# Kernel optimization log

Hardware: AMD Instinct MI355X
Metric: run time of the kernel (lower is better)

Reference implementation:

```python
import jax, jax.numpy as jnp
import numpy as np

B, S, E, H = 4, 1024, 768, 8
HD = E // H
FF = 4 * E
SCALING = HD ** -0.5


def _layernorm(x, g, b, eps=1e-5):
    m = jnp.mean(x, axis=-1, keepdims=True)
    v = jnp.var(x, axis=-1, keepdims=True)
    return (x - m) / jnp.sqrt(v + eps) * g + b


def setup_inputs() -> dict:
    key = jax.random.key(0)
    ks = jax.random.split(key, 12)
    w = lambda k, shp: (jax.random.normal(k, shp, jnp.float32) * 0.02)
    return {
        "x": jax.random.normal(ks[0], (B, S, E), jnp.float32),
        "dist_map": jax.random.uniform(ks[1], (B, H, S, S), jnp.float32),
        "mask": jnp.zeros((B, S), jnp.int32),
        "Wq": w(ks[2], (E, E)), "bq": jnp.zeros((E,), jnp.float32),
        "Wk": w(ks[3], (E, E)), "bk": jnp.zeros((E,), jnp.float32),
        "Wv": w(ks[4], (E, E)), "bv": jnp.zeros((E,), jnp.float32),
        "Wo": w(ks[5], (E, E)), "bo": jnp.zeros((E,), jnp.float32),
        "ln1_g": jnp.ones((E,), jnp.float32), "ln1_b": jnp.zeros((E,), jnp.float32),
        "W1": w(ks[6], (FF, E)), "b1": jnp.zeros((FF,), jnp.float32),
        "W2": w(ks[7], (E, FF)), "b2": jnp.zeros((E,), jnp.float32),
        "ln2_g": jnp.ones((E,), jnp.float32), "ln2_b": jnp.zeros((E,), jnp.float32),
    }


def reference(x, dist_map, mask, Wq, bq, Wk, bk, Wv, bv, Wo, bo,
              ln1_g, ln1_b, W1, b1, W2, b2, ln2_g, ln2_b):
    # --- attention residual block (pre-norm) ---
    h = _layernorm(x, ln1_g, ln1_b)
    # NOTE: torch does .view(B, H, S, HD) directly on [B, S, E] -> pure reshape, no transpose
    q = (h @ Wq.T + bq).reshape(B, H, S, HD)
    k = (h @ Wk.T + bk).reshape(B, H, S, HD)
    v = (h @ Wv.T + bv).reshape(B, H, S, HD)
    attn_weights = jnp.einsum("bhqd,bhkd->bhqk", q, k)
    pad = mask.astype(bool)[:, None, None, :]          # [B,1,1,S]
    attn_weights = jnp.where(pad, -10000.0, attn_weights)  # mask BEFORE scaling (as in source)
    probs = jax.nn.softmax(attn_weights * SCALING, axis=-1)
    probs = (probs + dist_map) * 0.5                   # post-softmax dist bias
    ctx = jnp.einsum("bhal,bhlv->bhav", probs, v)      # [B,H,S,HD]
    ctx = ctx.transpose(0, 2, 1, 3).reshape(B, S, E)
    x1 = x + (ctx @ Wo.T + bo)
    # --- FFN residual block (pre-norm) ---
    h2 = _layernorm(x1, ln2_g, ln2_b)
    ffn = jax.nn.gelu(h2 @ W1.T + b1, approximate=False) @ W2.T + b2
    out = x1 + ffn
    return out, probs
```

## Files before the change

kernel.cpp:

```cpp
#include <hip/hip_runtime.h>
#include <math.h>

typedef unsigned short u16;
typedef u16   u16x8  __attribute__((ext_vector_type(8)));
typedef u16   u16x4  __attribute__((ext_vector_type(4)));
typedef __bf16 bf16x8 __attribute__((ext_vector_type(8)));
typedef float f32x4  __attribute__((ext_vector_type(4)));

#define SZ_BSE   3145728
#define HEADSZ   98304
#define SCALING  0.10206207261596577f

__device__ __forceinline__ u16 f2bf(float f) {
  union { float f; unsigned u; } c; c.f = f;
  unsigned u = c.u;
  return (u16)((u + 0x7fffu + ((u >> 16) & 1u)) >> 16);
}

typedef const __attribute__((address_space(1))) unsigned int* gas1_t;
typedef __attribute__((address_space(3))) unsigned int* las3_t;
__device__ __forceinline__ void gload16(const void* g, void* l) {
  __builtin_amdgcn_global_load_lds((gas1_t)g, (las3_t)l, 16, 0, 0);
}

__global__ __launch_bounds__(256) void cvt_k(const float* __restrict__ in,
                                             u16* __restrict__ out, int n) {
  int i = (blockIdx.x * 256 + threadIdx.x) * 4;
  if (i >= n) return;
  f32x4 v = *(const f32x4*)&in[i];
  u16x4 o; o[0]=f2bf(v[0]); o[1]=f2bf(v[1]); o[2]=f2bf(v[2]); o[3]=f2bf(v[3]);
  *(u16x4*)&out[i] = o;
}

__global__ __launch_bounds__(256) void ln_k(const float* __restrict__ x,
                                            const float* __restrict__ g,
                                            const float* __restrict__ b,
                                            u16* __restrict__ out) {
  const int row = blockIdx.x;
  const float* xr = x + (long)row * 768;
  const int t = threadIdx.x;
  float v0 = xr[t], v1 = xr[t + 256], v2 = xr[t + 512];
  float s = v0 + v1 + v2, ss = v0*v0 + v1*v1 + v2*v2;
  for (int o = 32; o > 0; o >>= 1) { s += __shfl_xor(s, o); ss += __shfl_xor(ss, o); }
  __shared__ float red[8];
  int w = t >> 6;
  if ((t & 63) == 0) { red[w] = s; red[w + 4] = ss; }
  __syncthreads();
  s  = red[0] + red[1] + red[2] + red[3];
  ss = red[4] + red[5] + red[6] + red[7];
  float mean = s * (1.0f / 768.0f);
  float var  = ss * (1.0f / 768.0f) - mean * mean;
  float rstd = rsqrtf(var + 1e-5f);
  u16* orow = out + (long)row * 768;
  orow[t]       = f2bf((v0 - mean) * rstd * g[t]       + b[t]);
  orow[t + 256] = f2bf((v1 - mean) * rstd * g[t + 256] + b[t + 256]);
  orow[t + 512] = f2bf((v2 - mean) * rstd * g[t + 512] + b[t + 512]);
}

__global__ __launch_bounds__(256) void softmax_k(float* __restrict__ sc,
                                                 const float* __restrict__ dist) {
  const long row = blockIdx.x;
  float* sr = sc + row * 1024;
  const float* dr = dist + row * 1024;
  const int t = threadIdx.x;
  f32x4 x = *(const f32x4*)&sr[t * 4];
  x[0] *= SCALING; x[1] *= SCALING; x[2] *= SCALING; x[3] *= SCALING;
  float m = fmaxf(fmaxf(x[0], x[1]), fmaxf(x[2], x[3]));
  for (int o = 32; o > 0; o >>= 1) m = fmaxf(m, __shfl_xor(m, o));
  __shared__ float red[8];
  int w = t >> 6;
  if ((t & 63) == 0) red[w] = m;
  __syncthreads();
  m = fmaxf(fmaxf(red[0], red[1]), fmaxf(red[2], red[3]));
  f32x4 e;
  e[0] = expf(x[0] - m); e[1] = expf(x[1] - m);
  e[2] = expf(x[2] - m); e[3] = expf(x[3] - m);
  float s = e[0] + e[1] + e[2] + e[3];
  for (int o = 32; o > 0; o >>= 1) s += __shfl_xor(s, o);
  if ((t & 63) == 0) red[w + 4] = s;
  __syncthreads();
  s = red[4] + red[5] + red[6] + red[7];
  float inv = 1.0f / s;
  f32x4 d = *(const f32x4*)&dr[t * 4];
  f32x4 o4;
  o4[0] = (e[0] * inv + d[0]) * 0.5f;
  o4[1] = (e[1] * inv + d[1]) * 0.5f;
  o4[2] = (e[2] * inv + d[2]) * 0.5f;
  o4[3] = (e[3] * inv + d[3]) * 0.5f;
  *(f32x4*)&sr[t * 4] = o4;
}

__global__ __launch_bounds__(256) void vtrans_k(const u16* __restrict__ v,
                                                u16* __restrict__ vt) {
  __shared__ u16 tile[64 * 98];
  const int z = blockIdx.x >> 4;
  const int s0 = (blockIdx.x & 15) << 6;
  const int t = threadIdx.x;
  const u16* src = v + (long)z * HEADSZ + (long)s0 * 96;
#pragma unroll
  for (int it = 0; it < 3; ++it) {
    int i = it * 2048 + t * 8;
    int s = i / 96, d = i % 96;
    *(u16x8*)&tile[s * 98 + d] = *(const u16x8*)&src[i];
  }
  __syncthreads();
  u16* dst = vt + (long)z * HEADSZ + s0;
#pragma unroll
  for (int it = 0; it < 6; ++it) {
    int o = it * 1024 + t * 4;
    int d = o >> 6, s = o & 63;
    u16x4 wv;
#pragma unroll
    for (int j = 0; j < 4; ++j) wv[j] = tile[(s + j) * 98 + d];
    *(u16x4*)&dst[(long)d * 1024 + s] = wv;
  }
}

__global__ __launch_bounds__(256) void reduce_k(const float* __restrict__ p,
                                                const float* __restrict__ resid,
                                                const float* __restrict__ bias,
                                                float* __restrict__ out) {
  long i = ((long)blockIdx.x * 256 + threadIdx.x) * 4;
  f32x4 a = *(const f32x4*)&p[i];
  f32x4 b = *(const f32x4*)&p[3145728 + i];
  f32x4 c = *(const f32x4*)&p[6291456 + i];
  f32x4 r = *(const f32x4*)&resid[i];
  int cb = (int)(i % 768);
  f32x4 g = *(const f32x4*)&bias[cb];
  f32x4 o;
  o[0] = r[0] + g[0] + a[0] + b[0] + c[0];
  o[1] = r[1] + g[1] + a[1] + b[1] + c[1];
  o[2] = r[2] + g[2] + a[2] + b[2] + c[2];
  o[3] = r[3] + g[3] + a[3] + b[3] + c[3];
  *(f32x4*)&out[i] = o;
}

enum { EPI_QKV = 0, EPI_SCORES = 1, EPI_PV = 2, EPI_GELU = 3, EPI_PARTIAL = 4 };

template <int EPI, bool AF32>
__global__ __launch_bounds__(256, 2)
void gemm_k(const void* __restrict__ Av, long sAz, int lda,
            const u16* __restrict__ W, long sWz, int ldw,
            void* __restrict__ Cv, long sCz, int ldc,
            const float* __restrict__ bias,
            const int* __restrict__ mask,
            int N, int K, int kchunks) {
  __shared__ u16 sA[4096];
  __shared__ u16 sB[4096];

  const int t  = threadIdx.x;
  const int z  = blockIdx.z;
  const int bz = z / kchunks;
  const int kc = z - bz * kchunks;
  const int klen = K / kchunks;
  const int kbeg = kc * klen, kend = kbeg + klen;
  const int m0 = blockIdx.x * 128;
  const int n0 = blockIdx.y * 128;

  const int r0 = t >> 2;
  const int c0 = (t & 3) << 3;
  char* lA = (char*)sA + ((t >> 6) << 10);
  char* lB = (char*)sB + ((t >> 6) << 10);

  int bn0 = n0 + r0;      if (bn0 > N - 1) bn0 = N - 1;
  int bn1 = n0 + 64 + r0; if (bn1 > N - 1) bn1 = N - 1;
  const u16* Wz  = W + (long)bz * sWz;
  const u16* gB0 = Wz + (long)bn0 * ldw + c0;
  const u16* gB1 = Wz + (long)bn1 * ldw + c0;

  const u16*   Ab = AF32 ? nullptr : (const u16*)Av + (long)bz * sAz;
  const float* Af = AF32 ? (const float*)Av + (long)bz * sAz : nullptr;
  const u16* gA0 = AF32 ? nullptr : Ab + (long)(m0 + r0) * lda + c0;
  const u16* gA1 = AF32 ? nullptr : gA0 + 64 * lda;
  const float* Ap = AF32 ? Af + (long)(m0 + (t >> 1)) * lda + ((t & 1) << 4) : nullptr;
  u16* aw = &sA[(t >> 1) * 32 + ((t & 1) << 4)];

  const int lane = t & 63;
  const int w  = t >> 6;
  const int wm = (w >> 1) * 64, wn = (w & 1) * 64;
  const int lr = lane & 15, lg = lane >> 4;

  f32x4 acc[4][4] = {};

  for (int k0 = kbeg; k0 < kend; k0 += 32) {
    if (AF32) {
      f32x4 a0 = *(const f32x4*)(Ap + k0);
      f32x4 a1 = *(const f32x4*)(Ap + k0 + 4);
      f32x4 a2 = *(const f32x4*)(Ap + k0 + 8);
      f32x4 a3 = *(const f32x4*)(Ap + k0 + 12);
      u16x8 p0, p1;
      p0[0]=f2bf(a0[0]); p0[1]=f2bf(a0[1]); p0[2]=f2bf(a0[2]); p0[3]=f2bf(a0[3]);
      p0[4]=f2bf(a1[0]); p0[5]=f2bf(a1[1]); p0[6]=f2bf(a1[2]); p0[7]=f2bf(a1[3]);
      p1[0]=f2bf(a2[0]); p1[1]=f2bf(a2[1]); p1[2]=f2bf(a2[2]); p1[3]=f2bf(a2[3]);
      p1[4]=f2bf(a3[0]); p1[5]=f2bf(a3[1]); p1[6]=f2bf(a3[2]); p1[7]=f2bf(a3[3]);
      *(u16x8*)aw       = p0;
      *(u16x8*)(aw + 8) = p1;
    } else {
      gload16(gA0 + k0, lA);
      gload16(gA1 + k0, lA + 4096);
    }
    gload16(gB0 + k0, lB);
    gload16(gB1 + k0, lB + 4096);
    __syncthreads();

    bf16x8 aF[4], bF[4];
#pragma unroll
    for (int mi = 0; mi < 4; ++mi)
      aF[mi] = *(const bf16x8*)&sA[(wm + mi * 16 + lr) * 32 + lg * 8];
#pragma unroll
    for (int ni = 0; ni < 4; ++ni)
      bF[ni] = *(const bf16x8*)&sB[(wn + ni * 16 + lr) * 32 + lg * 8];
#pragma unroll
    for (int mi = 0; mi < 4; ++mi)
#pragma unroll
      for (int ni = 0; ni < 4; ++ni)
        acc[mi][ni] = __builtin_amdgcn_mfma_f32_16x16x32_bf16(aF[mi], bF[ni], acc[mi][ni], 0, 0, 0);
    __syncthreads();
  }

  long coff;
  if (EPI == EPI_PV)           coff = (long)(bz >> 3) * 786432 + (long)(bz & 7) * 96;
  else if (EPI == EPI_PARTIAL) coff = (long)kc * sCz;
  else                         coff = (long)bz * sCz;

#pragma unroll
  for (int mi = 0; mi < 4; ++mi) {
#pragma unroll
    for (int ni = 0; ni < 4; ++ni) {
      int gc = n0 + wn + ni * 16 + lr;
      if (gc >= N) continue;
      int gr0 = m0 + wm + mi * 16 + lg * 4;
#pragma unroll
      for (int r = 0; r < 4; ++r) {
        float vv = acc[mi][ni][r];
        long idx = coff + (long)(gr0 + r) * ldc + gc;
        if (EPI == EPI_QKV) {
          vv += bias[gc];
          int wsel = gc >= 1536 ? 2 : (gc >= 768 ? 1 : 0);
          int c = gc - wsel * 768;
          ((u16*)Cv)[(long)wsel * 3145728 + (long)(gr0 + r) * 768 + c] = f2bf(vv);
        } else if (EPI == EPI_SCORES) {
          if (mask[(bz >> 3) * 1024 + gc] != 0) vv = -10000.0f;
          ((float*)Cv)[idx] = vv;
        } else if (EPI == EPI_PV) {
          ((u16*)Cv)[idx] = f2bf(vv);
        } else if (EPI == EPI_GELU) {
          vv += bias[gc];
          vv = 0.5f * vv * (1.0f + erff(vv * 0.70710678118654752f));
          ((u16*)Cv)[idx] = f2bf(vv);
        } else {
          ((float*)Cv)[idx] = vv;
        }
      }
    }
  }
}

extern "C" void kernel_launch(void* const* d_in, const int* in_sizes, int n_in,
                              void* d_out, int out_size, void* d_ws, size_t ws_size,
                              hipStream_t stream) {
  (void)in_sizes; (void)n_in; (void)out_size; (void)ws_size;
  const float* x    = (const float*)d_in[0];
  const float* dist = (const float*)d_in[1];
  const int*   mask = (const int*)d_in[2];
  const float* Wq = (const float*)d_in[3];  const float* bq  = (const float*)d_in[4];
  const float* Wk = (const float*)d_in[5];  const float* bk  = (const float*)d_in[6];
  const float* Wv = (const float*)d_in[7];  const float* bv  = (const float*)d_in[8];
  const float* Wo = (const float*)d_in[9];  const float* bo  = (const float*)d_in[10];
  const float* g1 = (const float*)d_in[11]; const float* b1n = (const float*)d_in[12];
  const float* W1 = (const float*)d_in[13]; const float* b1f = (const float*)d_in[14];
  const float* W2 = (const float*)d_in[15]; const float* b2f = (const float*)d_in[16];
  const float* g2 = (const float*)d_in[17]; const float* b2n = (const float*)d_in[18];

  char* ws = (char*)d_ws;
  u16*   h    = (u16*)(ws + 0);
  u16*   ctx  = (u16*)(ws + 0);
  u16*   qkv  = (u16*)(ws + 6291456);
  u16*   q    = qkv;
  u16*   k    = (u16*)(ws + 12582912);
  u16*   v    = (u16*)(ws + 18874368);
  u16*   vT   = (u16*)(ws + 25165824);
  float* part = (float*)(ws + 6291456);
  u16*   h2   = (u16*)(ws + 31457280);
  u16*   ffn1 = (u16*)(ws + 44040192);
  float* x1   = (float*)(ws + 69206016);
  u16*   wqkvb= (u16*)(ws + 81788928);
  u16*   wob  = (u16*)(ws + 85327872);
  u16*   w1b  = (u16*)(ws + 86507520);
  u16*   w2b  = (u16*)(ws + 91226112);
  float* bqkv = (float*)(ws + 95944704);

  float* outp   = (float*)d_out;
  float* scores = outp + SZ_BSE;

  cvt_k<<<576,  256, 0, stream>>>(Wq, wqkvb,           589824);
  cvt_k<<<576,  256, 0, stream>>>(Wk, wqkvb + 589824,  589824);
  cvt_k<<<576,  256, 0, stream>>>(Wv, wqkvb + 1179648, 589824);
  cvt_k<<<576,  256, 0, stream>>>(Wo, wob, 589824);
  cvt_k<<<2304, 256, 0, stream>>>(W1, w1b, 2359296);
  cvt_k<<<2304, 256, 0, stream>>>(W2, w2b, 2359296);
  hipMemcpyAsync(bqkv,        bq, 3072, hipMemcpyDeviceToDevice, stream);
  hipMemcpyAsync(bqkv + 768,  bk, 3072, hipMemcpyDeviceToDevice, stream);
  hipMemcpyAsync(bqkv + 1536, bv, 3072, hipMemcpyDeviceToDevice, stream);

  ln_k<<<4096, 256, 0, stream>>>(x, g1, b1n, h);

  gemm_k<EPI_QKV, false><<<dim3(32, 18, 1), 256, 0, stream>>>(
      h, 0, 768, wqkvb, 0, 768, qkv, 0, 768, bqkv, nullptr, 2304, 768, 1);

  vtrans_k<<<512, 256, 0, stream>>>(v, vT);

  gemm_k<EPI_SCORES, false><<<dim3(8, 8, 32), 256, 0, stream>>>(
      q, HEADSZ, 96, k, HEADSZ, 96, scores, 1048576, 1024, nullptr, mask, 1024, 96, 1);

  softmax_k<<<32768, 256, 0, stream>>>(scores, dist);

  gemm_k<EPI_PV, true><<<dim3(8, 1, 32), 256, 0, stream>>>(
      scores, 1048576, 1024, vT, HEADSZ, 1024, ctx, 0, 768, nullptr, nullptr, 96, 1024, 1);

  gemm_k<EPI_PARTIAL, false><<<dim3(32, 6, 3), 256, 0, stream>>>(
      ctx, 0, 768, wob, 0, 768, part, 3145728, 768, nullptr, nullptr, 768, 768, 3);
  reduce_k<<<3072, 256, 0, stream>>>(part, x, bo, x1);

  ln_k<<<4096, 256, 0, stream>>>(x1, g2, b2n, h2);

  gemm_k<EPI_GELU, false><<<dim3(32, 24, 1), 256, 0, stream>>>(
      h2, 0, 768, w1b, 0, 768, ffn1, 0, 3072, b1f, nullptr, 3072, 768, 1);

  gemm_k<EPI_PARTIAL, false><<<dim3(32, 6, 3), 256, 0, stream>>>(
      ffn1, 0, 3072, w2b, 0, 3072, part, 3145728, 768, nullptr, nullptr, 768, 3072, 3);
  reduce_k<<<3072, 256, 0, stream>>>(part, x1, b2f, outp);
}
```

Before: 324.2 us.

## Fuse scores, softmax, dist bias and PV into a two-pass attention kernel

```diff
diff --git a/kernel.cpp b/kernel.cpp
--- a/kernel.cpp
+++ b/kernel.cpp
@@ -57,39 +57,6 @@
   orow[t + 512] = f2bf((v2 - mean) * rstd * g[t + 512] + b[t + 512]);
 }
 
-__global__ __launch_bounds__(256) void softmax_k(float* __restrict__ sc,
-                                                 const float* __restrict__ dist) {
-  const long row = blockIdx.x;
-  float* sr = sc + row * 1024;
-  const float* dr = dist + row * 1024;
-  const int t = threadIdx.x;
-  f32x4 x = *(const f32x4*)&sr[t * 4];
-  x[0] *= SCALING; x[1] *= SCALING; x[2] *= SCALING; x[3] *= SCALING;
-  float m = fmaxf(fmaxf(x[0], x[1]), fmaxf(x[2], x[3]));
-  for (int o = 32; o > 0; o >>= 1) m = fmaxf(m, __shfl_xor(m, o));
-  __shared__ float red[8];
-  int w = t >> 6;
-  if ((t & 63) == 0) red[w] = m;
-  __syncthreads();
-  m = fmaxf(fmaxf(red[0], red[1]), fmaxf(red[2], red[3]));
-  f32x4 e;
-  e[0] = expf(x[0] - m); e[1] = expf(x[1] - m);
-  e[2] = expf(x[2] - m); e[3] = expf(x[3] - m);
-  float s = e[0] + e[1] + e[2] + e[3];
-  for (int o = 32; o > 0; o >>= 1) s += __shfl_xor(s, o);
-  if ((t & 63) == 0) red[w + 4] = s;
-  __syncthreads();
-  s = red[4] + red[5] + red[6] + red[7];
-  float inv = 1.0f / s;
-  f32x4 d = *(const f32x4*)&dr[t * 4];
-  f32x4 o4;
-  o4[0] = (e[0] * inv + d[0]) * 0.5f;
-  o4[1] = (e[1] * inv + d[1]) * 0.5f;
-  o4[2] = (e[2] * inv + d[2]) * 0.5f;
-  o4[3] = (e[3] * inv + d[3]) * 0.5f;
-  *(f32x4*)&sr[t * 4] = o4;
-}
-
 __global__ __launch_bounds__(256) void vtrans_k(const u16* __restrict__ v,
                                                 u16* __restrict__ vt) {
   __shared__ u16 tile[64 * 98];
@@ -135,23 +102,162 @@
   *(f32x4*)&out[i] = o;
 }
 
-enum { EPI_QKV = 0, EPI_SCORES = 1, EPI_PV = 2, EPI_GELU = 3, EPI_PARTIAL = 4 };
-
-template <int EPI, bool AF32>
 __global__ __launch_bounds__(256, 2)
-void gemm_k(const void* __restrict__ Av, long sAz, int lda,
-            const u16* __restrict__ W, long sWz, int ldw,
+void attn_k(const u16* __restrict__ qb, const u16* __restrict__ kb,
+            const u16* __restrict__ vT, const float* __restrict__ dist,
+            const int* __restrict__ maskp, float* __restrict__ probs,
+            u16* __restrict__ ctx) {
+  __shared__ u16 sP[64 * 88];
+  __shared__ u16 sFlag[1024];
+
+  const int t = threadIdx.x;
+  const int z = blockIdx.y;
+  const int r0 = blockIdx.x * 64;
+  const int b = z >> 3, h = z & 7;
+
+  {
+    const int* mp = maskp + b * 1024 + t * 4;
+    int4 mv = *(const int4*)mp;
+    sFlag[t*4+0] = (u16)(mv.x != 0);
+    sFlag[t*4+1] = (u16)(mv.y != 0);
+    sFlag[t*4+2] = (u16)(mv.z != 0);
+    sFlag[t*4+3] = (u16)(mv.w != 0);
+  }
+  __syncthreads();
+
+  const int lane = t & 63;
+  const int w = t >> 6;
+  const int wr0 = w * 16;
+  const int lr = lane & 15;
+  const int lg = lane >> 4;
+
+  const u16* qh = qb + (long)z * HEADSZ;
+  const u16* kh = kb + (long)z * HEADSZ;
+  const u16* vh = vT + (long)z * HEADSZ;
+  const float* dh = dist + (long)z * 1048576;
+  float* ph = probs + (long)z * 1048576;
+
+  bf16x8 qa[3];
+  {
+    const u16* qr = qh + (long)(r0 + wr0 + lr) * 96 + lg * 8;
+#pragma unroll
+    for (int kf = 0; kf < 3; ++kf) qa[kf] = *(const bf16x8*)(qr + kf * 32);
+  }
+
+  const float neg = -10000.0f * SCALING;
+  float mrun[4] = {-3.0e38f, -3.0e38f, -3.0e38f, -3.0e38f};
+  float srun[4] = {0.f, 0.f, 0.f, 0.f};
+
+  for (int c = 0; c < 16; ++c) {
+    const int c0 = c * 64;
+    f32x4 a4[4] = {};
+#pragma unroll
+    for (int ni = 0; ni < 4; ++ni) {
+      const u16* kr = kh + (long)(c0 + ni * 16 + lr) * 96 + lg * 8;
+#pragma unroll
+      for (int kf = 0; kf < 3; ++kf)
+        a4[ni] = __builtin_amdgcn_mfma_f32_16x16x32_bf16(
+            qa[kf], *(const bf16x8*)(kr + kf * 32), a4[ni], 0, 0, 0);
+    }
+    f32x4 ssc[4];
+#pragma unroll
+    for (int ni = 0; ni < 4; ++ni) {
+      bool fm = sFlag[c0 + ni * 16 + lr] != 0;
+#pragma unroll
+      for (int r = 0; r < 4; ++r)
+        ssc[ni][r] = fm ? neg : a4[ni][r] * SCALING;
+    }
+#pragma unroll
+    for (int r = 0; r < 4; ++r) {
+      float cm = fmaxf(fmaxf(ssc[0][r], ssc[1][r]), fmaxf(ssc[2][r], ssc[3][r]));
+      cm = fmaxf(cm, __shfl_xor(cm, 1));
+      cm = fmaxf(cm, __shfl_xor(cm, 2));
+      cm = fmaxf(cm, __shfl_xor(cm, 4));
+      cm = fmaxf(cm, __shfl_xor(cm, 8));
+      float mnew = fmaxf(mrun[r], cm);
+      float cs = expf(ssc[0][r] - mnew) + expf(ssc[1][r] - mnew)
+               + expf(ssc[2][r] - mnew) + expf(ssc[3][r] - mnew);
+      cs += __shfl_xor(cs, 1);
+      cs += __shfl_xor(cs, 2);
+      cs += __shfl_xor(cs, 4);
+      cs += __shfl_xor(cs, 8);
+      srun[r] = srun[r] * expf(mrun[r] - mnew) + cs;
+      mrun[r] = mnew;
+    }
+  }
+  float inv[4];
+#pragma unroll
+  for (int r = 0; r < 4; ++r) inv[r] = 1.0f / srun[r];
+
+  f32x4 cacc[6] = {};
+  for (int c = 0; c < 16; ++c) {
+    const int c0 = c * 64;
+    f32x4 dv[4];
+#pragma unroll
+    for (int ni = 0; ni < 4; ++ni) {
+      const float* dp = dh + (long)(r0 + wr0 + lg * 4) * 1024 + c0 + ni * 16 + lr;
+#pragma unroll
+      for (int r = 0; r < 4; ++r) dv[ni][r] = dp[r * 1024];
+    }
+    f32x4 a4[4] = {};
+#pragma unroll
+    for (int ni = 0; ni < 4; ++ni) {
+      const u16* kr = kh + (long)(c0 + ni * 16 + lr) * 96 + lg * 8;
+#pragma unroll
+      for (int kf = 0; kf < 3; ++kf)
+        a4[ni] = __builtin_amdgcn_mfma_f32_16x16x32_bf16(
+            qa[kf], *(const bf16x8*)(kr + kf * 32), a4[ni], 0, 0, 0);
+    }
+#pragma unroll
+    for (int ni = 0; ni < 4; ++ni) {
+      bool fm = sFlag[c0 + ni * 16 + lr] != 0;
+      float* pp = ph + (long)(r0 + wr0 + lg * 4) * 1024 + c0 + ni * 16 + lr;
+      int sb = (wr0 + lg * 4) * 88 + ni * 16 + lr;
+#pragma unroll
+      for (int r = 0; r < 4; ++r) {
+        float sv = fm ? neg : a4[ni][r] * SCALING;
+        float e = expf(sv - mrun[r]) * inv[r];
+        float pr = (e + dv[ni][r]) * 0.5f;
+        pp[r * 1024] = pr;
+        sP[sb + r * 88] = f2bf(pr);
+      }
+    }
+#pragma unroll
+    for (int ks = 0; ks < 2; ++ks) {
+      bf16x8 pa = *(const bf16x8*)&sP[(wr0 + lr) * 88 + ks * 32 + lg * 8];
+      const u16* vr = vh + (long)lr * 1024 + c0 + ks * 32 + lg * 8;
+#pragma unroll
+      for (int n2 = 0; n2 < 6; ++n2) {
+        bf16x8 vb = *(const bf16x8*)(vr + (long)n2 * 16 * 1024);
+        cacc[n2] = __builtin_amdgcn_mfma_f32_16x16x32_bf16(pa, vb, cacc[n2], 0, 0, 0);
+      }
+    }
+  }
+
+  u16* cbase = ctx + (long)b * 786432 + h * 96;
+#pragma unroll
+  for (int n2 = 0; n2 < 6; ++n2) {
+    int d = n2 * 16 + lr;
+#pragma unroll
+    for (int r = 0; r < 4; ++r)
+      cbase[(long)(r0 + wr0 + lg * 4 + r) * 768 + d] = f2bf(cacc[n2][r]);
+  }
+}
+
+enum { EPI_QKV = 0, EPI_GELU = 1, EPI_PARTIAL = 2 };
+
+template <int EPI>
+__global__ __launch_bounds__(256, 2)
+void gemm_k(const u16* __restrict__ A, int lda,
+            const u16* __restrict__ W, int ldw,
             void* __restrict__ Cv, long sCz, int ldc,
             const float* __restrict__ bias,
-            const int* __restrict__ mask,
             int N, int K, int kchunks) {
   __shared__ u16 sA[4096];
   __shared__ u16 sB[4096];
 
   const int t  = threadIdx.x;
-  const int z  = blockIdx.z;
-  const int bz = z / kchunks;
-  const int kc = z - bz * kchunks;
+  const int kc = blockIdx.z;
   const int klen = K / kchunks;
   const int kbeg = kc * klen, kend = kbeg + klen;
   const int m0 = blockIdx.x * 128;
@@ -164,16 +270,10 @@
 
   int bn0 = n0 + r0;      if (bn0 > N - 1) bn0 = N - 1;
   int bn1 = n0 + 64 + r0; if (bn1 > N - 1) bn1 = N - 1;
-  const u16* Wz  = W + (long)bz * sWz;
-  const u16* gB0 = Wz + (long)bn0 * ldw + c0;
-  const u16* gB1 = Wz + (long)bn1 * ldw + c0;
-
-  const u16*   Ab = AF32 ? nullptr : (const u16*)Av + (long)bz * sAz;
-  const float* Af = AF32 ? (const float*)Av + (long)bz * sAz : nullptr;
-  const u16* gA0 = AF32 ? nullptr : Ab + (long)(m0 + r0) * lda + c0;
-  const u16* gA1 = AF32 ? nullptr : gA0 + 64 * lda;
-  const float* Ap = AF32 ? Af + (long)(m0 + (t >> 1)) * lda + ((t & 1) << 4) : nullptr;
-  u16* aw = &sA[(t >> 1) * 32 + ((t & 1) << 4)];
+  const u16* gB0 = W + (long)bn0 * ldw + c0;
+  const u16* gB1 = W + (long)bn1 * ldw + c0;
+  const u16* gA0 = A + (long)(m0 + r0) * lda + c0;
+  const u16* gA1 = gA0 + 64 * lda;
 
   const int lane = t & 63;
   const int w  = t >> 6;
@@ -183,22 +283,8 @@
   f32x4 acc[4][4] = {};
 
   for (int k0 = kbeg; k0 < kend; k0 += 32) {
-    if (AF32) {
-      f32x4 a0 = *(const f32x4*)(Ap + k0);
-      f32x4 a1 = *(const f32x4*)(Ap + k0 + 4);
-      f32x4 a2 = *(const f32x4*)(Ap + k0 + 8);
-      f32x4 a3 = *(const f32x4*)(Ap + k0 + 12);
-      u16x8 p0, p1;
-      p0[0]=f2bf(a0[0]); p0[1]=f2bf(a0[1]); p0[2]=f2bf(a0[2]); p0[3]=f2bf(a0[3]);
-      p0[4]=f2bf(a1[0]); p0[5]=f2bf(a1[1]); p0[6]=f2bf(a1[2]); p0[7]=f2bf(a1[3]);
-      p1[0]=f2bf(a2[0]); p1[1]=f2bf(a2[1]); p1[2]=f2bf(a2[2]); p1[3]=f2bf(a2[3]);
-      p1[4]=f2bf(a3[0]); p1[5]=f2bf(a3[1]); p1[6]=f2bf(a3[2]); p1[7]=f2bf(a3[3]);
-      *(u16x8*)aw       = p0;
-      *(u16x8*)(aw + 8) = p1;
-    } else {
-      gload16(gA0 + k0, lA);
-      gload16(gA1 + k0, lA + 4096);
-    }
+    gload16(gA0 + k0, lA);
+    gload16(gA1 + k0, lA + 4096);
     gload16(gB0 + k0, lB);
     gload16(gB1 + k0, lB + 4096);
     __syncthreads();
@@ -218,10 +304,7 @@
     __syncthreads();
   }
 
-  long coff;
-  if (EPI == EPI_PV)           coff = (long)(bz >> 3) * 786432 + (long)(bz & 7) * 96;
-  else if (EPI == EPI_PARTIAL) coff = (long)kc * sCz;
-  else                         coff = (long)bz * sCz;
+  long coff = (EPI == EPI_PARTIAL) ? (long)kc * sCz : 0;
 
 #pragma unroll
   for (int mi = 0; mi < 4; ++mi) {
@@ -233,23 +316,17 @@
 #pragma unroll
       for (int r = 0; r < 4; ++r) {
         float vv = acc[mi][ni][r];
-        long idx = coff + (long)(gr0 + r) * ldc + gc;
         if (EPI == EPI_QKV) {
           vv += bias[gc];
           int wsel = gc >= 1536 ? 2 : (gc >= 768 ? 1 : 0);
           int c = gc - wsel * 768;
           ((u16*)Cv)[(long)wsel * 3145728 + (long)(gr0 + r) * 768 + c] = f2bf(vv);
-        } else if (EPI == EPI_SCORES) {
-          if (mask[(bz >> 3) * 1024 + gc] != 0) vv = -10000.0f;
-          ((float*)Cv)[idx] = vv;
-        } else if (EPI == EPI_PV) {
-          ((u16*)Cv)[idx] = f2bf(vv);
         } else if (EPI == EPI_GELU) {
           vv += bias[gc];
           vv = 0.5f * vv * (1.0f + erff(vv * 0.70710678118654752f));
-          ((u16*)Cv)[idx] = f2bf(vv);
+          ((u16*)Cv)[coff + (long)(gr0 + r) * ldc + gc] = f2bf(vv);
         } else {
-          ((float*)Cv)[idx] = vv;
+          ((float*)Cv)[coff + (long)(gr0 + r) * ldc + gc] = vv;
         }
       }
     }
@@ -291,7 +368,7 @@
   float* bqkv = (float*)(ws + 95944704);
 
   float* outp   = (float*)d_out;
-  float* scores = outp + SZ_BSE;
+  float* probs  = outp + SZ_BSE;
 
   cvt_k<<<576,  256, 0, stream>>>(Wq, wqkvb,           589824);
   cvt_k<<<576,  256, 0, stream>>>(Wk, wqkvb + 589824,  589824);
@@ -305,29 +382,23 @@
 
   ln_k<<<4096, 256, 0, stream>>>(x, g1, b1n, h);
 
-  gemm_k<EPI_QKV, false><<<dim3(32, 18, 1), 256, 0, stream>>>(
-      h, 0, 768, wqkvb, 0, 768, qkv, 0, 768, bqkv, nullptr, 2304, 768, 1);
+  gemm_k<EPI_QKV><<<dim3(32, 18, 1), 256, 0, stream>>>(
+      h, 768, wqkvb, 768, qkv, 0, 768, bqkv, 2304, 768, 1);
 
   vtrans_k<<<512, 256, 0, stream>>>(v, vT);
 
-  gemm_k<EPI_SCORES, false><<<dim3(8, 8, 32), 256, 0, stream>>>(
-      q, HEADSZ, 96, k, HEADSZ, 96, scores, 1048576, 1024, nullptr, mask, 1024, 96, 1);
-
-  softmax_k<<<32768, 256, 0, stream>>>(scores, dist);
-
-  gemm_k<EPI_PV, true><<<dim3(8, 1, 32), 256, 0, stream>>>(
-      scores, 1048576, 1024, vT, HEADSZ, 1024, ctx, 0, 768, nullptr, nullptr, 96, 1024, 1);
-
-  gemm_k<EPI_PARTIAL, false><<<dim3(32, 6, 3), 256, 0, stream>>>(
-      ctx, 0, 768, wob, 0, 768, part, 3145728, 768, nullptr, nullptr, 768, 768, 3);
+  attn_k<<<dim3(16, 32), 256, 0, stream>>>(q, k, vT, dist, mask, probs, ctx);
+
+  gemm_k<EPI_PARTIAL><<<dim3(32, 6, 3), 256, 0, stream>>>(
+      ctx, 768, wob, 768, part, 3145728, 768, nullptr, 768, 768, 3);
   reduce_k<<<3072, 256, 0, stream>>>(part, x, bo, x1);
 
   ln_k<<<4096, 256, 0, stream>>>(x1, g2, b2n, h2);
 
-  gemm_k<EPI_GELU, false><<<dim3(32, 24, 1), 256, 0, stream>>>(
-      h2, 0, 768, w1b, 0, 768, ffn1, 0, 3072, b1f, nullptr, 3072, 768, 1);
-
-  gemm_k<EPI_PARTIAL, false><<<dim3(32, 6, 3), 256, 0, stream>>>(
-      ffn1, 0, 3072, w2b, 0, 3072, part, 3145728, 768, nullptr, nullptr, 768, 3072, 3);
+  gemm_k<EPI_GELU><<<dim3(32, 24, 1), 256, 0, stream>>>(
+      h2, 768, w1b, 768, ffn1, 0, 3072, b1f, 3072, 768, 1);
+
+  gemm_k<EPI_PARTIAL><<<dim3(32, 6, 3), 256, 0, stream>>>(
+      ffn1, 3072, w2b, 3072, part, 3145728, 768, nullptr, 768, 3072, 3);
   reduce_k<<<3072, 256, 0, stream>>>(part, x1, b2f, outp);
 }
```

Measured after the change: 366.2 us. 13.0% more time.
